# Performance work log

Measured on AMD Instinct MI355X. Metric: run time of the kernel, lower is better.

Reference implementation:

```python
import jax, jax.numpy as jnp
import numpy as np

T, M = 64, 64
ROI, SPA, WORD, I3D = 2048, 4, 300, 1024
H, D = 512, 256  # so_hidden, so_out_dim (= rel_dim)
IN = ROI + SPA + WORD  # 2352


def _w(k, shape):
    return jax.random.normal(k, shape, dtype=jnp.float32) * 0.02


def setup_inputs() -> dict:
    key = jax.random.key(0)
    ks = jax.random.split(key, 32)
    inp = {
        "roi_feats": jax.random.normal(ks[0], (T, M, ROI), dtype=jnp.float32),
        "spatial": jax.random.uniform(ks[1], (T, M, SPA), dtype=jnp.float32),
        "i3d_feats": jax.random.normal(ks[2], (T, I3D), dtype=jnp.float32),
        "subj_emb": jax.random.normal(ks[3], (WORD,), dtype=jnp.float32),
        "obj_emb": jax.random.normal(ks[4], (WORD,), dtype=jnp.float32),
        "pred_emb": jax.random.normal(ks[5], (WORD,), dtype=jnp.float32),
        # subject / object encoders (torch Linear convention: W is (out,in))
        "subj_w1": _w(ks[6], (H, IN)), "subj_b1": _w(ks[7], (H,)),
        "subj_w2": _w(ks[8], (D, H)), "subj_b2": _w(ks[9], (D,)),
        "obj_w1": _w(ks[10], (H, IN)), "obj_b1": _w(ks[11], (H,)),
        "obj_w2": _w(ks[12], (D, H)), "obj_b2": _w(ks[13], (D,)),
        # fuse MLPs (in = 2*D)
        "fuse_s_w1": _w(ks[14], (H, 2 * D)), "fuse_s_b1": _w(ks[15], (H,)),
        "fuse_s_w2": _w(ks[16], (D, H)), "fuse_s_b2": _w(ks[17], (D,)),
        "fuse_o_w1": _w(ks[18], (H, 2 * D)), "fuse_o_b1": _w(ks[19], (H,)),
        "fuse_o_w2": _w(ks[20], (D, H)), "fuse_o_b2": _w(ks[21], (D,)),
        # relation projections + MLP
        "W_rs": _w(ks[22], (D, D)),
        "W_ro": _w(ks[23], (D, D)),
        "rel_w1": _w(ks[24], (H, D + WORD)), "rel_b1": _w(ks[25], (H,)),
        "rel_w2": _w(ks[26], (D, H)), "rel_b2": _w(ks[27], (D,)),
    }
    return inp


def _linear(x, W, b):
    return x @ W.T + b


def _mlp2(x, w1, b1, w2, b2):
    return _linear(jax.nn.relu(_linear(x, w1, b1)), w2, b2)


def reference(roi_feats, spatial, i3d_feats, subj_emb, obj_emb, pred_emb,
              subj_w1, subj_b1, subj_w2, subj_b2,
              obj_w1, obj_b1, obj_w2, obj_b2,
              fuse_s_w1, fuse_s_b1, fuse_s_w2, fuse_s_b2,
              fuse_o_w1, fuse_o_b1, fuse_o_w2, fuse_o_b2,
              W_rs, W_ro, rel_w1, rel_b1, rel_w2, rel_b2):
    Tn, Mn, _ = roi_feats.shape
    se = jnp.broadcast_to(subj_emb, (Tn, Mn, subj_emb.shape[-1]))
    oe = jnp.broadcast_to(obj_emb, (Tn, Mn, obj_emb.shape[-1]))
    # SubjectObjectEncoder: fc2(relu(fc1([roi; spa; word])))
    fs_base = _mlp2(jnp.concatenate([roi_feats, spatial, se], axis=-1),
                    subj_w1, subj_b1, subj_w2, subj_b2)  # (T,M,D)
    fo_base = _mlp2(jnp.concatenate([roi_feats, spatial, oe], axis=-1),
                    obj_w1, obj_b1, obj_w2, obj_b2)
    # use_gsa = use_lla = False -> fuse([base; base])
    fs = _mlp2(jnp.concatenate([fs_base, fs_base], axis=-1),
               fuse_s_w1, fuse_s_b1, fuse_s_w2, fuse_s_b2)
    fo = _mlp2(jnp.concatenate([fo_base, fo_base], axis=-1),
               fuse_o_w1, fuse_o_b1, fuse_o_w2, fuse_o_b2)
    # Eq. 15: pairwise diff + predicate word, then 2-layer MLP
    fs_proj = fs @ W_rs.T
    fo_proj = fo @ W_ro.T
    diff = fs_proj[:, :, None, :] - fo_proj[:, None, :, :]  # (T,M,M,D)
    # rel_fc1([diff; pred]) split into diff part + constant pred part
    Wd, Wp = rel_w1[:, :fs.shape[-1]], rel_w1[:, fs.shape[-1]:]
    h = jax.nn.relu(diff @ Wd.T + (pred_emb @ Wp.T + rel_b1))  # (T,M,M,H)
    return h @ rel_w2.T + rel_b2  # (T,M,M,D)
```

## Files before the change

### kernel.cpp

```cpp
#include <hip/hip_runtime.h>
#include <hip/hip_bf16.h>

typedef __attribute__((ext_vector_type(4))) float f32x4;
typedef __attribute__((ext_vector_type(8))) short s16x8;

__device__ __forceinline__ void async_lds16(const void* g, void* l) {
  __builtin_amdgcn_global_load_lds((const __attribute__((address_space(1))) void*)g,
                                   (__attribute__((address_space(3))) void*)l, 16, 0, 0);
}

__device__ __forceinline__ short f2bf(float x) {
  __hip_bfloat16 h = __float2bfloat16(x);
  short s;
  __builtin_memcpy(&s, &h, 2);
  return s;
}

__device__ __forceinline__ s16x8 pack8(f32x4 a, f32x4 b) {
  s16x8 r;
  r[0] = f2bf(a[0]); r[1] = f2bf(a[1]); r[2] = f2bf(a[2]); r[3] = f2bf(a[3]);
  r[4] = f2bf(b[0]); r[5] = f2bf(b[1]); r[6] = f2bf(b[2]); r[7] = f2bf(b[3]);
  return r;
}

template<bool RELU, bool OUT_BF16, bool HAS_BIAS>
__global__ __launch_bounds__(256) void gemm_bt(
    const __hip_bfloat16* __restrict__ Ag, const __hip_bfloat16* __restrict__ Bg,
    const float* __restrict__ biasg, void* __restrict__ Cg,
    int lda, int ldb, int K, int ldc,
    int strideA, int strideB, int strideBias, long strideC)
{
  __shared__ __align__(16) short As[4096];
  __shared__ __align__(16) short Bs[4096];
  const int tid  = threadIdx.x;
  const int lane = tid & 63;
  const int wid  = tid >> 6;
  const int z    = blockIdx.z;
  const __hip_bfloat16* A = Ag + (long)z * strideA;
  const __hip_bfloat16* B = Bg + (long)z * strideB;
  const float* bias = HAS_BIAS ? (biasg + (long)z * strideBias) : nullptr;
  const int row0 = blockIdx.y * 128;
  const int col0 = blockIdx.x * 128;

  const int srow = wid * 16 + (lane >> 2);
  const int scol = (lane & 3) * 8;

  f32x4 acc[4][4];
#pragma unroll
  for (int i = 0; i < 4; ++i)
#pragma unroll
    for (int j = 0; j < 4; ++j) acc[i][j] = (f32x4)(0.0f);

  const int rw = (wid & 1) * 64;
  const int cw = (wid >> 1) * 64;
  const int lm = lane & 15;
  const int kg = (lane >> 4) * 8;

  for (int ks = 0; ks < K; ks += 32) {
    __syncthreads();
#pragma unroll
    for (int is = 0; is < 2; ++is) {
      async_lds16(A + (long)(row0 + is * 64 + srow) * lda + ks + scol,
                  (char*)As + is * 4096 + wid * 1024);
      async_lds16(B + (long)(col0 + is * 64 + srow) * ldb + ks + scol,
                  (char*)Bs + is * 4096 + wid * 1024);
    }
    __syncthreads();
    s16x8 af[4], bf[4];
#pragma unroll
    for (int mt = 0; mt < 4; ++mt)
      af[mt] = *(const s16x8*)(As + (rw + mt * 16 + lm) * 32 + kg);
#pragma unroll
    for (int nt = 0; nt < 4; ++nt)
      bf[nt] = *(const s16x8*)(Bs + (cw + nt * 16 + lm) * 32 + kg);
#pragma unroll
    for (int mt = 0; mt < 4; ++mt)
#pragma unroll
      for (int nt = 0; nt < 4; ++nt)
        acc[mt][nt] = __builtin_amdgcn_mfma_f32_16x16x32_bf16(af[mt], bf[nt], acc[mt][nt], 0, 0, 0);
  }

  const int lr4 = (lane >> 4) * 4;
#pragma unroll
  for (int mt = 0; mt < 4; ++mt) {
#pragma unroll
    for (int nt = 0; nt < 4; ++nt) {
      const int col = col0 + cw + nt * 16 + lm;
      const float bv = HAS_BIAS ? bias[col] : 0.0f;
#pragma unroll
      for (int r = 0; r < 4; ++r) {
        const int row = row0 + rw + mt * 16 + lr4 + r;
        float v = acc[mt][nt][r] + bv;
        if (RELU) v = fmaxf(v, 0.0f);
        if (OUT_BF16)
          ((__hip_bfloat16*)Cg)[(long)z * strideC + (long)row * ldc + col] = __float2bfloat16(v);
        else
          ((float*)Cg)[(long)z * strideC + (long)row * ldc + col] = v;
      }
    }
  }
}

template<bool RELU, bool OUT_BF16, bool HAS_BIAS>
__global__ __launch_bounds__(256) void gemm_bt64(
    const __hip_bfloat16* __restrict__ Ag, const __hip_bfloat16* __restrict__ Bg,
    const float* __restrict__ biasg, void* __restrict__ Cg,
    int lda, int ldb, int K, int ldc,
    int strideA, int strideB, int strideBias, long strideC)
{
  __shared__ __align__(16) short As[2048];
  __shared__ __align__(16) short Bs[2048];
  const int tid  = threadIdx.x;
  const int lane = tid & 63;
  const int wid  = tid >> 6;
  const int z    = blockIdx.z;
  const __hip_bfloat16* A = Ag + (long)z * strideA;
  const __hip_bfloat16* B = Bg + (long)z * strideB;
  const float* bias = HAS_BIAS ? (biasg + (long)z * strideBias) : nullptr;
  const int row0 = blockIdx.y * 64;
  const int col0 = blockIdx.x * 64;

  const int srow = wid * 16 + (lane >> 2);
  const int scol = (lane & 3) * 8;

  f32x4 acc[2][2];
#pragma unroll
  for (int i = 0; i < 2; ++i)
#pragma unroll
    for (int j = 0; j < 2; ++j) acc[i][j] = (f32x4)(0.0f);

  const int rw = (wid & 1) * 32;
  const int cw = (wid >> 1) * 32;
  const int lm = lane & 15;
  const int kg = (lane >> 4) * 8;

  for (int ks = 0; ks < K; ks += 32) {
    __syncthreads();
    async_lds16(A + (long)(row0 + srow) * lda + ks + scol, (char*)As + wid * 1024);
    async_lds16(B + (long)(col0 + srow) * ldb + ks + scol, (char*)Bs + wid * 1024);
    __syncthreads();
    s16x8 af[2], bf[2];
#pragma unroll
    for (int mt = 0; mt < 2; ++mt)
      af[mt] = *(const s16x8*)(As + (rw + mt * 16 + lm) * 32 + kg);
#pragma unroll
    for (int nt = 0; nt < 2; ++nt)
      bf[nt] = *(const s16x8*)(Bs + (cw + nt * 16 + lm) * 32 + kg);
#pragma unroll
    for (int mt = 0; mt < 2; ++mt)
#pragma unroll
      for (int nt = 0; nt < 2; ++nt)
        acc[mt][nt] = __builtin_amdgcn_mfma_f32_16x16x32_bf16(af[mt], bf[nt], acc[mt][nt], 0, 0, 0);
  }

  const int lr4 = (lane >> 4) * 4;
#pragma unroll
  for (int mt = 0; mt < 2; ++mt) {
#pragma unroll
    for (int nt = 0; nt < 2; ++nt) {
      const int col = col0 + cw + nt * 16 + lm;
      const float bv = HAS_BIAS ? bias[col] : 0.0f;
#pragma unroll
      for (int r = 0; r < 4; ++r) {
        const int row = row0 + rw + mt * 16 + lr4 + r;
        float v = acc[mt][nt][r] + bv;
        if (RELU) v = fmaxf(v, 0.0f);
        if (OUT_BF16)
          ((__hip_bfloat16*)Cg)[(long)z * strideC + (long)row * ldc + col] = __float2bfloat16(v);
        else
          ((float*)Cg)[(long)z * strideC + (long)row * ldc + col] = v;
      }
    }
  }
}

__global__ __launch_bounds__(256) void reduce_relu(
    const float* __restrict__ P, const float* __restrict__ cboth,
    __hip_bfloat16* __restrict__ H1)
{
  const int id = blockIdx.x * 256 + threadIdx.x;
  const int row = id >> 7, c8 = id & 127;
  const f32x4* p0 = (const f32x4*)(P + (long)row * 1024 + c8 * 8);
  const f32x4* p1 = (const f32x4*)(P + 4194304 + (long)row * 1024 + c8 * 8);
  const f32x4* bb = (const f32x4*)(cboth + c8 * 8);
  f32x4 a = p0[0] + p1[0] + bb[0];
  f32x4 b = p0[1] + p1[1] + bb[1];
#pragma unroll
  for (int e = 0; e < 4; ++e) { a[e] = fmaxf(a[e], 0.0f); b[e] = fmaxf(b[e], 0.0f); }
  *(s16x8*)((short*)H1 + (long)row * 1024 + c8 * 8) = pack8(a, b);
}

__global__ __launch_bounds__(256) void rel_final(
    const float* __restrict__ AsBo, const __hip_bfloat16* __restrict__ W2b,
    const float* __restrict__ b2, float* __restrict__ out)
{
  __shared__ __align__(16) short Hs[4096];
  __shared__ __align__(16) short Ws[8192];
  const int tid  = threadIdx.x;
  const int lane = tid & 63;
  const int wid  = tid >> 6;
  const int i0 = blockIdx.x * 2;
  const int t  = blockIdx.y;

  const float* Ap = AsBo + (long)(t * 64 + i0) * 512;
  const float* Bp = AsBo + 2097152 + (long)t * 64 * 512;

  const int grow = tid >> 1;
  const int gkc  = (tid & 1) * 16;
  const float* arow = Ap + (grow >> 6) * 512 + gkc;
  const float* brow = Bp + (grow & 63) * 512 + gkc;
  const int hbyte = (grow * 64 + (tid & 1) * 32) ^ ((grow & 7) << 4);

  const int wsrow = lane >> 2;
  const int wscol = (lane & 3) * 8;

  f32x4 acc[4][8];
#pragma unroll
  for (int i = 0; i < 4; ++i)
#pragma unroll
    for (int j = 0; j < 8; ++j) acc[i][j] = (f32x4)(0.0f);

  const int rw = (wid & 1) * 64;
  const int cw = (wid >> 1) * 128;
  const int lm = lane & 15;
  const int kg = (lane >> 4) * 8;
  const int hrbase = (lm * 64 + kg * 2) ^ ((lm & 7) << 4);

  for (int ks = 0; ks < 512; ks += 32) {
    __syncthreads();
#pragma unroll
    for (int q = 0; q < 4; ++q)
      async_lds16(W2b + (long)(wid * 64 + q * 16 + wsrow) * 512 + ks + wscol,
                  (char*)Ws + wid * 4096 + q * 1024);
    f32x4 av[4], bv[4];
#pragma unroll
    for (int q = 0; q < 4; ++q) {
      av[q] = *(const f32x4*)(arow + ks + q * 4);
      bv[q] = *(const f32x4*)(brow + ks + q * 4);
    }
    union { s16x8 v; short s[8]; } p0, p1;
#pragma unroll
    for (int q = 0; q < 2; ++q)
#pragma unroll
      for (int e = 0; e < 4; ++e) {
        p0.s[q * 4 + e] = f2bf(fmaxf(av[q][e] - bv[q][e], 0.0f));
        p1.s[q * 4 + e] = f2bf(fmaxf(av[q + 2][e] - bv[q + 2][e], 0.0f));
      }
    *(s16x8*)((char*)Hs + hbyte) = p0.v;
    *(s16x8*)((char*)Hs + (hbyte ^ 16)) = p1.v;
    __syncthreads();
    s16x8 af[4], bf[8];
#pragma unroll
    for (int mt = 0; mt < 4; ++mt)
      af[mt] = *(const s16x8*)((char*)Hs + (rw + mt * 16) * 64 + hrbase);
#pragma unroll
    for (int nt = 0; nt < 8; ++nt)
      bf[nt] = *(const s16x8*)(Ws + (cw + nt * 16 + lm) * 32 + kg);
#pragma unroll
    for (int mt = 0; mt < 4; ++mt)
#pragma unroll
      for (int nt = 0; nt < 8; ++nt)
        acc[mt][nt] = __builtin_amdgcn_mfma_f32_16x16x32_bf16(af[mt], bf[nt], acc[mt][nt], 0, 0, 0);
  }

  const int lr4 = (lane >> 4) * 4;
  const long obase = (long)(t * 64 + i0) * 64 * 256;
#pragma unroll
  for (int mt = 0; mt < 4; ++mt) {
#pragma unroll
    for (int nt = 0; nt < 8; ++nt) {
      const int col = cw + nt * 16 + lm;
      const float bvv = b2[col];
#pragma unroll
      for (int r = 0; r < 4; ++r) {
        const int prow = rw + mt * 16 + lr4 + r;
        const int il = prow >> 6, j = prow & 63;
        out[obase + (long)(il * 64 + j) * 256 + col] = acc[mt][nt][r] + bvv;
      }
    }
  }
}

__global__ __launch_bounds__(256) void prep_kernel(
    const float* __restrict__ roi, const float* __restrict__ spatial,
    const float* __restrict__ subj_emb, const float* __restrict__ obj_emb,
    const float* __restrict__ pred_emb,
    const float* __restrict__ subj_w1, const float* __restrict__ subj_b1,
    const float* __restrict__ obj_w1, const float* __restrict__ obj_b1,
    const float* __restrict__ subj_w2, const float* __restrict__ subj_b2,
    const float* __restrict__ obj_w2, const float* __restrict__ obj_b2,
    const float* __restrict__ fs_w1, const float* __restrict__ fs_b1,
    const float* __restrict__ fs_w2, const float* __restrict__ fs_b2,
    const float* __restrict__ fo_w1, const float* __restrict__ fo_b1,
    const float* __restrict__ fo_w2, const float* __restrict__ fo_b2,
    const float* __restrict__ W_rs, const float* __restrict__ W_ro,
    const float* __restrict__ rel_w1, const float* __restrict__ rel_b1,
    const float* __restrict__ rel_w2,
    __hip_bfloat16* __restrict__ XP, __hip_bfloat16* __restrict__ W1P,
    float* __restrict__ cboth,
    __hip_bfloat16* __restrict__ Bcat2, float* __restrict__ bias2,
    __hip_bfloat16* __restrict__ WfCat, float* __restrict__ biasf,
    __hip_bfloat16* __restrict__ W4cat, float* __restrict__ bias4,
    __hip_bfloat16* __restrict__ WcCat, float* __restrict__ crel,
    __hip_bfloat16* __restrict__ W2b)
{
  int id = blockIdx.x * 256 + threadIdx.x;

  if (id < 1081344) {
    int row = id / 264, c8 = id - row * 264;
    s16x8 o;
    if (c8 < 256) {
      const f32x4* src = (const f32x4*)(roi + (long)row * 2048 + c8 * 8);
      o = pack8(src[0], src[1]);
    } else {
      f32x4 a, b;
#pragma unroll
      for (int e = 0; e < 4; ++e) {
        int col = c8 * 8 + e;
        a[e] = (col < 2052) ? spatial[row * 4 + (col - 2048)] : 0.0f;
        int col2 = col + 4;
        b[e] = (col2 < 2052) ? spatial[row * 4 + (col2 - 2048)] : 0.0f;
      }
      o = pack8(a, b);
    }
    *(s16x8*)((short*)XP + (long)id * 8) = o;
    return;
  }
  id -= 1081344;
  if (id < 270336) {
    int row = id / 264, c8 = id - row * 264;
    const float* w = (row < 512) ? (subj_w1 + (long)row * 2352)
                                 : (obj_w1 + (long)(row - 512) * 2352);
    s16x8 o;
    if (c8 < 256) {
      const f32x4* src = (const f32x4*)(w + c8 * 8);
      o = pack8(src[0], src[1]);
    } else {
      f32x4 a, b;
#pragma unroll
      for (int e = 0; e < 4; ++e) {
        int col = c8 * 8 + e;
        a[e] = (col < 2052) ? w[col] : 0.0f;
        int col2 = col + 4;
        b[e] = (col2 < 2052) ? w[col2] : 0.0f;
      }
      o = pack8(a, b);
    }
    *(s16x8*)((short*)W1P + (long)id * 8) = o;
    return;
  }
  id -= 270336;
  if (id < 1024) {
    int h = id;
    const float* w; const float* e; float s;
    if (h < 512) { w = subj_w1 + (long)h * 2352 + 2052; e = subj_emb; s = subj_b1[h]; }
    else { w = obj_w1 + (long)(h - 512) * 2352 + 2052; e = obj_emb; s = obj_b1[h - 512]; }
    for (int k = 0; k < 300; ++k) s += w[k] * e[k];
    cboth[h] = s;
    return;
  }
  id -= 1024;
  if (id < 32768) {
    const float* src = (id < 16384) ? (subj_w2 + id * 8) : (obj_w2 + (id - 16384) * 8);
    const f32x4* s4 = (const f32x4*)src;
    *(s16x8*)((short*)Bcat2 + (long)id * 8) = pack8(s4[0], s4[1]);
    return;
  }
  id -= 32768;
  if (id < 512) { bias2[id] = (id < 256) ? subj_b2[id] : obj_b2[id - 256]; return; }
  id -= 512;
  if (id < 32768) {
    int z = id >> 14, r8 = id & 16383;
    int h = r8 >> 5, d8 = r8 & 31;
    const float* w = (z ? fo_w1 : fs_w1) + h * 512 + d8 * 8;
    const f32x4* lo = (const f32x4*)w;
    const f32x4* hi = (const f32x4*)(w + 256);
    *(s16x8*)((short*)WfCat + (long)id * 8) = pack8(lo[0] + hi[0], lo[1] + hi[1]);
    return;
  }
  id -= 32768;
  if (id < 1024) { biasf[id] = (id < 512) ? fs_b1[id] : fo_b1[id - 512]; return; }
  id -= 1024;
  if (id < 32768) {
    const float* src = (id < 16384) ? (fs_w2 + id * 8) : (fo_w2 + (id - 16384) * 8);
    const f32x4* s4 = (const f32x4*)src;
    *(s16x8*)((short*)W4cat + (long)id * 8) = pack8(s4[0], s4[1]);
    return;
  }
  id -= 32768;
  if (id < 512) { bias4[id] = (id < 256) ? fs_b2[id] : fo_b2[id - 256]; return; }
  id -= 512;
  if (id < 262144) {
    int z = id >> 17, r = id & 131071;
    int h = r >> 8, d = r & 255;
    const float* Wr = z ? W_ro : W_rs;
    const float* wd = rel_w1 + (long)h * 556;
    float s = 0.0f;
    for (int e = 0; e < 256; ++e) s += wd[e] * Wr[e * 256 + d];
    WcCat[id] = __float2bfloat16(s);
    return;
  }
  id -= 262144;
  if (id < 1024) {
    int z = id >> 9, h = id & 511;
    float s = 0.0f;
    if (z == 0) {
      s = rel_b1[h];
      const float* wp = rel_w1 + (long)h * 556 + 256;
      for (int k = 0; k < 300; ++k) s += pred_emb[k] * wp[k];
    }
    crel[id] = s;
    return;
  }
  id -= 1024;
  if (id < 16384) {
    const f32x4* s4 = (const f32x4*)(rel_w2 + id * 8);
    *(s16x8*)((short*)W2b + (long)id * 8) = pack8(s4[0], s4[1]);
  }
}

extern "C" void kernel_launch(void* const* d_in, const int* in_sizes, int n_in,
                              void* d_out, int out_size, void* d_ws, size_t ws_size,
                              hipStream_t stream)
{
  const float* roi       = (const float*)d_in[0];
  const float* spatial   = (const float*)d_in[1];
  const float* subj_emb  = (const float*)d_in[3];
  const float* obj_emb   = (const float*)d_in[4];
  const float* pred_emb  = (const float*)d_in[5];
  const float* subj_w1   = (const float*)d_in[6];
  const float* subj_b1   = (const float*)d_in[7];
  const float* subj_w2   = (const float*)d_in[8];
  const float* subj_b2   = (const float*)d_in[9];
  const float* obj_w1    = (const float*)d_in[10];
  const float* obj_b1    = (const float*)d_in[11];
  const float* obj_w2    = (const float*)d_in[12];
  const float* obj_b2    = (const float*)d_in[13];
  const float* fuse_s_w1 = (const float*)d_in[14];
  const float* fuse_s_b1 = (const float*)d_in[15];
  const float* fuse_s_w2 = (const float*)d_in[16];
  const float* fuse_s_b2 = (const float*)d_in[17];
  const float* fuse_o_w1 = (const float*)d_in[18];
  const float* fuse_o_b1 = (const float*)d_in[19];
  const float* fuse_o_w2 = (const float*)d_in[20];
  const float* fuse_o_b2 = (const float*)d_in[21];
  const float* W_rs      = (const float*)d_in[22];
  const float* W_ro      = (const float*)d_in[23];
  const float* rel_w1    = (const float*)d_in[24];
  const float* rel_b1    = (const float*)d_in[25];
  const float* rel_w2    = (const float*)d_in[26];
  const float* rel_b2    = (const float*)d_in[27];

  char* ws = (char*)d_ws;
  __hip_bfloat16* XP   = (__hip_bfloat16*)(ws);
  float*          AsBo = (float*)(ws);
  __hip_bfloat16* W1P  = (__hip_bfloat16*)(ws + 17301504);
  __hip_bfloat16* H1   = (__hip_bfloat16*)(ws + 21626880);
  __hip_bfloat16* FS   = (__hip_bfloat16*)(ws + 30015488);
  float*          P    = (float*)(ws + 34209792);
  const size_t so = 67764224;
  __hip_bfloat16* Bcat2 = (__hip_bfloat16*)(ws + so);
  float*          bias2 = (float*)(ws + so + 524288);
  __hip_bfloat16* WfCat = (__hip_bfloat16*)(ws + so + 526336);
  float*          biasf = (float*)(ws + so + 1050624);
  __hip_bfloat16* W4cat = (__hip_bfloat16*)(ws + so + 1054720);
  float*          bias4 = (float*)(ws + so + 1579008);
  __hip_bfloat16* WcCat = (__hip_bfloat16*)(ws + so + 1581056);
  float*          crel  = (float*)(ws + so + 2105344);
  __hip_bfloat16* W2b   = (__hip_bfloat16*)(ws + so + 2109440);
  float*          cboth = (float*)(ws + so + 2371584);

  prep_kernel<<<6768, 256, 0, stream>>>(
      roi, spatial, subj_emb, obj_emb, pred_emb,
      subj_w1, subj_b1, obj_w1, obj_b1, subj_w2, subj_b2, obj_w2, obj_b2,
      fuse_s_w1, fuse_s_b1, fuse_s_w2, fuse_s_b2,
      fuse_o_w1, fuse_o_b1, fuse_o_w2, fuse_o_b2,
      W_rs, W_ro, rel_w1, rel_b1, rel_w2,
      XP, W1P, cboth, Bcat2, bias2, WfCat, biasf, W4cat, bias4, WcCat, crel, W2b);

  gemm_bt<false, false, false><<<dim3(8, 32, 2), 256, 0, stream>>>(
      XP, W1P, cboth, P, 2112, 2112, 1056, 1024, 1056, 1056, 0, 4194304L);
  reduce_relu<<<2048, 256, 0, stream>>>(P, cboth, H1);
  gemm_bt64<false, true, true><<<dim3(4, 64, 2), 256, 0, stream>>>(
      H1, Bcat2, bias2, FS, 1024, 512, 512, 512, 512, 131072, 256, 256);
  gemm_bt64<true, true, true><<<dim3(8, 64, 2), 256, 0, stream>>>(
      FS, WfCat, biasf, H1, 512, 256, 256, 1024, 256, 131072, 512, 512);
  gemm_bt64<false, true, true><<<dim3(4, 64, 2), 256, 0, stream>>>(
      H1, W4cat, bias4, FS, 1024, 512, 512, 512, 512, 131072, 256, 256);
  gemm_bt64<false, false, true><<<dim3(8, 64, 2), 256, 0, stream>>>(
      FS, WcCat, crel, AsBo, 512, 256, 256, 512, 256, 131072, 512, 2097152L);
  rel_final<<<dim3(32, 64), 256, 0, stream>>>(AsBo, W2b, rel_b2, (float*)d_out);
}
```

Measured before the change: 630.7 us.

## Double-buffer LDS in rel_final and swizzle block order across XCDs

Converts the rel_final K-loop into a double-buffered pipeline: the next slice's weight async loads and activation global loads are issued before the current slice's MFMAs, and the relu-diff bf16 packing is written into the alternate buffer afterwards, so one barrier per iteration replaces two. It also raises wave priority around the MFMA block and remaps the 1D block index so consecutive blocks on the same XCD share a time step. The cost is doubled LDS (48KB) and extra registers held live across the MFMAs, which may lower occupancy.

```diff
diff --git a/kernel.cpp b/kernel.cpp
--- a/kernel.cpp
+++ b/kernel.cpp
@@ -194,13 +194,15 @@
     const float* __restrict__ AsBo, const __hip_bfloat16* __restrict__ W2b,
     const float* __restrict__ b2, float* __restrict__ out)
 {
-  __shared__ __align__(16) short Hs[4096];
-  __shared__ __align__(16) short Ws[8192];
+  __shared__ __align__(16) short Hs[2][4096];
+  __shared__ __align__(16) short Ws[2][8192];
   const int tid  = threadIdx.x;
   const int lane = tid & 63;
   const int wid  = tid >> 6;
-  const int i0 = blockIdx.x * 2;
-  const int t  = blockIdx.y;
+  const int bid = (int)blockIdx.x;
+  const int swz = (bid & 7) * 256 + (bid >> 3);
+  const int t  = swz >> 5;
+  const int i0 = (swz & 31) * 2;
 
   const float* Ap = AsBo + (long)(t * 64 + i0) * 512;
   const float* Bp = AsBo + 2097152 + (long)t * 64 * 512;
@@ -226,17 +228,16 @@
   const int kg = (lane >> 4) * 8;
   const int hrbase = (lm * 64 + kg * 2) ^ ((lm & 7) << 4);
 
-  for (int ks = 0; ks < 512; ks += 32) {
-    __syncthreads();
-#pragma unroll
-    for (int q = 0; q < 4; ++q)
-      async_lds16(W2b + (long)(wid * 64 + q * 16 + wsrow) * 512 + ks + wscol,
-                  (char*)Ws + wid * 4096 + q * 1024);
+#pragma unroll
+  for (int q = 0; q < 4; ++q)
+    async_lds16(W2b + (long)(wid * 64 + q * 16 + wsrow) * 512 + wscol,
+                (char*)Ws[0] + wid * 4096 + q * 1024);
+  {
     f32x4 av[4], bv[4];
 #pragma unroll
     for (int q = 0; q < 4; ++q) {
-      av[q] = *(const f32x4*)(arow + ks + q * 4);
-      bv[q] = *(const f32x4*)(brow + ks + q * 4);
+      av[q] = *(const f32x4*)(arow + q * 4);
+      bv[q] = *(const f32x4*)(brow + q * 4);
     }
     union { s16x8 v; short s[8]; } p0, p1;
 #pragma unroll
@@ -246,21 +247,54 @@
         p0.s[q * 4 + e] = f2bf(fmaxf(av[q][e] - bv[q][e], 0.0f));
         p1.s[q * 4 + e] = f2bf(fmaxf(av[q + 2][e] - bv[q + 2][e], 0.0f));
       }
-    *(s16x8*)((char*)Hs + hbyte) = p0.v;
-    *(s16x8*)((char*)Hs + (hbyte ^ 16)) = p1.v;
-    __syncthreads();
+    *(s16x8*)((char*)Hs[0] + hbyte) = p0.v;
+    *(s16x8*)((char*)Hs[0] + (hbyte ^ 16)) = p1.v;
+  }
+  __syncthreads();
+
+#pragma unroll
+  for (int it = 0; it < 16; ++it) {
+    const int cur = it & 1, nxt = cur ^ 1;
+    f32x4 av[4], bv[4];
+    if (it < 15) {
+      const int ks = (it + 1) * 32;
+#pragma unroll
+      for (int q = 0; q < 4; ++q)
+        async_lds16(W2b + (long)(wid * 64 + q * 16 + wsrow) * 512 + ks + wscol,
+                    (char*)Ws[nxt] + wid * 4096 + q * 1024);
+#pragma unroll
+      for (int q = 0; q < 4; ++q) {
+        av[q] = *(const f32x4*)(arow + ks + q * 4);
+        bv[q] = *(const f32x4*)(brow + ks + q * 4);
+      }
+    }
     s16x8 af[4], bf[8];
 #pragma unroll
     for (int mt = 0; mt < 4; ++mt)
-      af[mt] = *(const s16x8*)((char*)Hs + (rw + mt * 16) * 64 + hrbase);
+      af[mt] = *(const s16x8*)((char*)Hs[cur] + (rw + mt * 16) * 64 + hrbase);
 #pragma unroll
     for (int nt = 0; nt < 8; ++nt)
-      bf[nt] = *(const s16x8*)(Ws + (cw + nt * 16 + lm) * 32 + kg);
+      bf[nt] = *(const s16x8*)((short*)Ws[cur] + (cw + nt * 16 + lm) * 32 + kg);
+    __builtin_amdgcn_s_setprio(1);
 #pragma unroll
     for (int mt = 0; mt < 4; ++mt)
 #pragma unroll
       for (int nt = 0; nt < 8; ++nt)
         acc[mt][nt] = __builtin_amdgcn_mfma_f32_16x16x32_bf16(af[mt], bf[nt], acc[mt][nt], 0, 0, 0);
+    __builtin_amdgcn_s_setprio(0);
+    if (it < 15) {
+      union { s16x8 v; short s[8]; } p0, p1;
+#pragma unroll
+      for (int q = 0; q < 2; ++q)
+#pragma unroll
+        for (int e = 0; e < 4; ++e) {
+          p0.s[q * 4 + e] = f2bf(fmaxf(av[q][e] - bv[q][e], 0.0f));
+          p1.s[q * 4 + e] = f2bf(fmaxf(av[q + 2][e] - bv[q + 2][e], 0.0f));
+        }
+      *(s16x8*)((char*)Hs[nxt] + hbyte) = p0.v;
+      *(s16x8*)((char*)Hs[nxt] + (hbyte ^ 16)) = p1.v;
+    }
+    __syncthreads();
   }
 
   const int lr4 = (lane >> 4) * 4;
@@ -489,5 +523,5 @@
       H1, W4cat, bias4, FS, 1024, 512, 512, 512, 512, 131072, 256, 256);
   gemm_bt64<false, false, true><<<dim3(8, 64, 2), 256, 0, stream>>>(
       FS, WcCat, crel, AsBo, 512, 256, 256, 512, 256, 131072, 512, 2097152L);
-  rel_final<<<dim3(32, 64), 256, 0, stream>>>(AsBo, W2b, rel_b2, (float*)d_out);
-}
+  rel_final<<<2048, 256, 0, stream>>>(AsBo, W2b, rel_b2, (float*)d_out);
+}
```

Measured after the change: 616.9 us. 2.2% less time.
